# Kernel optimization log

Measured on AMD Instinct MI355X. Metric: run time of the kernel, lower is better.

The kernel has to match this reference:

```python
import jax, jax.numpy as jnp
import numpy as np

N_NODES = 256
BATCH = 1024
N_LAYERS = 2  # total linear layers = N_LAYERS + 1, each followed by tanh


def setup_inputs() -> dict:
    key = jax.random.key(0)
    ks = jax.random.split(key, 4)
    scale = 1.0 / np.sqrt(N_NODES)
    x = jax.random.normal(ks[0], (BATCH, N_NODES), dtype=jnp.float32)
    # nn.Linear weights: [out_features, in_features], no bias
    W0 = jax.random.normal(ks[1], (N_NODES, N_NODES), dtype=jnp.float32) * scale
    W1 = jax.random.normal(ks[2], (N_NODES, N_NODES), dtype=jnp.float32) * scale
    W2 = jax.random.normal(ks[3], (N_NODES, N_NODES), dtype=jnp.float32) * scale
    return {"x": x, "W0": W0, "W1": W1, "W2": W2}


def reference(x, W0, W1, W2):
    # Original loop: for each node i, zero out column i of x (x @ Par with
    # Par = I - e_i e_i^T), run the 3-layer tanh MLP, keep output column i.
    # Vectorized: build all N masked copies at once.
    N = x.shape[1]
    mask = (1.0 - jnp.eye(N, dtype=x.dtype))  # [i, j]: zero col j==i
    Xm = x[None, :, :] * mask[:, None, :]     # [N, B, N]
    # nn.Linear: y = h @ W.T ; tanh after every layer (incl. last)
    h = jnp.tanh(jnp.einsum('ibn,mn->ibm', Xm, W0))
    h = jnp.tanh(jnp.einsum('ibn,mn->ibm', h, W1))
    h = jnp.tanh(jnp.einsum('ibn,mn->ibm', h, W2))  # [N, B, N]
    # f_x[b, i] = h[i, b, i]
    f_x = jnp.einsum('ibi->bi', h)
    return f_x
```

## Files before the change

kernel.cpp:

```cpp
#include <hip/hip_runtime.h>
#include <hip/hip_bf16.h>

#define N_NODES 256
#define BATCH   1024
#define ROWB    528
#define CSC     2.8853900817779268f

typedef __attribute__((ext_vector_type(8))) short bf16x8;
typedef __attribute__((ext_vector_type(4))) float f32x4;
typedef __attribute__((ext_vector_type(2))) float f32x2;

__device__ __forceinline__ float ftanh(float x) {
    float e = __builtin_amdgcn_exp2f(x * CSC);
    float r = __builtin_amdgcn_rcpf(e + 1.0f);
    return fmaf(-2.0f, r, 1.0f);
}

__device__ __forceinline__ unsigned short f2bf(float f) {
    unsigned u = __float_as_uint(f);
    return (unsigned short)((u + 0x7fffu + ((u >> 16) & 1u)) >> 16);
}

__device__ __forceinline__ unsigned pack_bf2(float a, float b) {
    union { __hip_bfloat162 h; unsigned u; } cvt;
    cvt.h = __float22bfloat162_rn(make_float2(a, b));
    return cvt.u;
}

__device__ __forceinline__ f32x2 pkfma(f32x2 a, f32x2 b, f32x2 c) {
    return __builtin_elementwise_fma(a, b, c);
}

__device__ __forceinline__ f32x2 tanh2_pre(f32x2 d2) {
    f32x2 e2;
    e2.x = __builtin_amdgcn_exp2f(d2.x);
    e2.y = __builtin_amdgcn_exp2f(d2.y);
    e2 = e2 + 1.0f;
    f32x2 r2;
    r2.x = __builtin_amdgcn_rcpf(e2.x);
    r2.y = __builtin_amdgcn_rcpf(e2.y);
    return pkfma((f32x2){-2.f, -2.f}, r2, (f32x2){1.f, 1.f});
}

template <int CTRL>
__device__ __forceinline__ float dpp_add(float s) {
    int t = __builtin_amdgcn_update_dpp(0, __float_as_int(s), CTRL, 0xf, 0xf, true);
    return s + __int_as_float(t);
}

__global__ void z0_prep(const float* __restrict__ x, const float* __restrict__ W0,
                        const float* __restrict__ W1, float* __restrict__ Z0c,
                        float* __restrict__ xT, float* __restrict__ W0c,
                        unsigned short* __restrict__ W1bf) {
    __shared__ float xs[32][36];
    __shared__ float ws[32][36];
    int t = threadIdx.x;

    int gb = (blockIdx.y * 32 + blockIdx.x) * 256 + t;
    {
        int i = gb >> 8, m = gb & 255;
        W0c[gb]  = W0[m * 256 + i] * CSC;
        W1bf[gb] = f2bf(W1[gb] * CSC);
    }
#pragma unroll
    for (int r = 0; r < 4; ++r) {
        int id = r * 65536 + gb;
        int i = id >> 10, b = id & 1023;
        xT[id] = x[b * 256 + i];
    }

    int b0 = blockIdx.x * 32, m0 = blockIdx.y * 32;
    int lr = t >> 3, lc = (t & 7) << 2;
    int tr = (t >> 4) << 1, tc = (t & 15) << 1;
    float acc00 = 0.f, acc01 = 0.f, acc10 = 0.f, acc11 = 0.f;
    for (int k0 = 0; k0 < 256; k0 += 32) {
        *(float4*)&xs[lr][lc] = *(const float4*)&x[(b0 + lr) * 256 + k0 + lc];
        *(float4*)&ws[lr][lc] = *(const float4*)&W0[(m0 + lr) * 256 + k0 + lc];
        __syncthreads();
#pragma unroll
        for (int k = 0; k < 32; ++k) {
            float a0 = xs[tr][k], a1 = xs[tr + 1][k];
            float w0v = ws[tc][k], w1v = ws[tc + 1][k];
            acc00 = fmaf(a0, w0v, acc00);
            acc01 = fmaf(a0, w1v, acc01);
            acc10 = fmaf(a1, w0v, acc10);
            acc11 = fmaf(a1, w1v, acc11);
        }
        __syncthreads();
    }
    Z0c[(b0 + tr) * 256 + m0 + tc]         = acc00 * CSC;
    Z0c[(b0 + tr) * 256 + m0 + tc + 1]     = acc01 * CSC;
    Z0c[(b0 + tr + 1) * 256 + m0 + tc]     = acc10 * CSC;
    Z0c[(b0 + tr + 1) * 256 + m0 + tc + 1] = acc11 * CSC;
}

__launch_bounds__(256, 4)
__global__ void fused(const float* __restrict__ Z0c, const float* __restrict__ xT,
                      const float* __restrict__ W0c,
                      const unsigned short* __restrict__ W1bf,
                      const float* __restrict__ W2, float* __restrict__ out) {
    __shared__ __align__(16) unsigned char h0s[64 * ROWB];
    __shared__ float wavepart[4 * 64];
    const int t  = threadIdx.x;
    const int r0 = blockIdx.x * 64;
    const int i  = blockIdx.y;

    const int wave = t >> 6, lane = t & 63;
    const int lr = lane & 15, lh = lane >> 4;

    float w2v[4];
#pragma unroll
    for (int nt = 0; nt < 4; ++nt)
        w2v[nt] = W2[i * 256 + wave * 64 + nt * 16 + lr];

    {
        const int rowgrp = t >> 5, chunk = t & 31;
        const int col0 = chunk << 3;
        unsigned char* wbase = h0s + rowgrp * ROWB + chunk * 16;
        f32x2 wv[4];
        {
            float4 w0a = *(const float4*)&W0c[i * 256 + col0];
            float4 w0b = *(const float4*)&W0c[i * 256 + col0 + 4];
            wv[0] = (f32x2){w0a.x, w0a.y};
            wv[1] = (f32x2){w0a.z, w0a.w};
            wv[2] = (f32x2){w0b.x, w0b.y};
            wv[3] = (f32x2){w0b.z, w0b.w};
        }
#pragma unroll
        for (int p = 0; p < 8; ++p) {
            int row = p * 8 + rowgrp;
            float xi = xT[i * 1024 + r0 + row];
            f32x2 nxi = (f32x2){-xi, -xi};
            float4 za = *(const float4*)&Z0c[(r0 + row) * 256 + col0];
            float4 zb = *(const float4*)&Z0c[(r0 + row) * 256 + col0 + 4];
            f32x2 zv[4] = {(f32x2){za.x, za.y}, (f32x2){za.z, za.w},
                           (f32x2){zb.x, zb.y}, (f32x2){zb.z, zb.w}};
            unsigned pk[4];
#pragma unroll
            for (int e = 0; e < 4; ++e) {
                f32x2 h = tanh2_pre(pkfma(nxi, wv[e], zv[e]));
                pk[e] = pack_bf2(h.x, h.y);
            }
            *(uint4*)(wbase + p * 8 * ROWB) = make_uint4(pk[0], pk[1], pk[2], pk[3]);
        }
    }
    __syncthreads();

    f32x4 acc[4][4];
#pragma unroll
    for (int a = 0; a < 4; ++a)
#pragma unroll
        for (int b = 0; b < 4; ++b)
            acc[a][b] = (f32x4){0.f, 0.f, 0.f, 0.f};

    const unsigned char* abase[4];
#pragma unroll
    for (int mt = 0; mt < 4; ++mt)
        abase[mt] = h0s + (mt * 16 + lr) * ROWB + lh * 16;

    const unsigned short* w1p[4];
#pragma unroll
    for (int nt = 0; nt < 4; ++nt)
        w1p[nt] = W1bf + (wave * 64 + nt * 16 + lr) * 256 + lh * 8;
    bf16x8 bnext[4];
#pragma unroll
    for (int nt = 0; nt < 4; ++nt)
        bnext[nt] = *(const bf16x8*)(w1p[nt]);

#pragma unroll
    for (int ks = 0; ks < 8; ++ks) {
        bf16x8 bfrag[4];
#pragma unroll
        for (int nt = 0; nt < 4; ++nt) {
            bfrag[nt] = bnext[nt];
            if (ks < 7)
                bnext[nt] = *(const bf16x8*)(w1p[nt] + (ks + 1) * 32);
        }
        bf16x8 afrag[4];
#pragma unroll
        for (int mt = 0; mt < 4; ++mt)
            afrag[mt] = *(const bf16x8*)(abase[mt] + ks * 64);
#pragma unroll
        for (int mt = 0; mt < 4; ++mt)
#pragma unroll
            for (int nt = 0; nt < 4; ++nt)
                acc[mt][nt] = __builtin_amdgcn_mfma_f32_16x16x32_bf16(
                    afrag[mt], bfrag[nt], acc[mt][nt], 0, 0, 0);
    }

#pragma unroll
    for (int mt = 0; mt < 4; ++mt) {
#pragma unroll
        for (int p = 0; p < 2; ++p) {
            f32x2 s2 = (f32x2){0.f, 0.f};
#pragma unroll
            for (int nt = 0; nt < 4; ++nt) {
                f32x2 zc = (f32x2){acc[mt][nt][2 * p], acc[mt][nt][2 * p + 1]};
                f32x2 h2 = tanh2_pre(zc);
                s2 = pkfma(h2, (f32x2){w2v[nt], w2v[nt]}, s2);
            }
#pragma unroll
            for (int q = 0; q < 2; ++q) {
                float s = s2[q];
                s = dpp_add<0x118>(s);
                s = dpp_add<0x114>(s);
                s = dpp_add<0x112>(s);
                s = dpp_add<0x111>(s);
                if (lr == 15)
                    wavepart[wave * 64 + mt * 16 + lh * 4 + 2 * p + q] = s;
            }
        }
    }
    __syncthreads();

    if (t < 64) {
        float s = wavepart[t] + wavepart[64 + t] + wavepart[128 + t] + wavepart[192 + t];
        out[(r0 + t) * 256 + i] = ftanh(s);
    }
}

extern "C" void kernel_launch(void* const* d_in, const int* in_sizes, int n_in,
                              void* d_out, int out_size, void* d_ws, size_t ws_size,
                              hipStream_t stream) {
    const float* x  = (const float*)d_in[0];
    const float* W0 = (const float*)d_in[1];
    const float* W1 = (const float*)d_in[2];
    const float* W2 = (const float*)d_in[3];
    float* out = (float*)d_out;

    char* ws = (char*)d_ws;
    float* Z0c           = (float*)ws;
    float* xT            = (float*)(ws + (1 << 20));
    float* W0c           = (float*)(ws + (2 << 20));
    unsigned short* W1bf = (unsigned short*)(ws + (2 << 20) + (256 << 10));

    z0_prep<<<dim3(32, 8), 256, 0, stream>>>(x, W0, W1, Z0c, xT, W0c, W1bf);
    fused<<<dim3(16, 256), 256, 0, stream>>>(Z0c, xT, W0c, W1bf, W2, out);
}
```

Measured before the change: 87.78 us.

## Warp-specialize fused kernel: producer waves build h0 while MFMA waves consume

The fused kernel now processes 8 node indices per block with 512 threads. Four producer waves compute the tanh-masked first layer into a double-buffered LDS tile for the next index, while four consumer waves run the MFMA second layer and the reduction for the current index. The final output write for each index is deferred by one iteration. The goal is to overlap the elementwise/global-load phase with the matrix phase and to amortize block launch. The costs are more LDS per block, a block-wide barrier per index, and a lower occupancy bound.

```diff
diff --git a/kernel.cpp b/kernel.cpp
--- a/kernel.cpp
+++ b/kernel.cpp
@@ -3,6 +3,7 @@
 
 #define N_NODES 256
 #define BATCH   1024
+#define NI      8
 #define ROWB    528
 #define CSC     2.8853900817779268f
 
@@ -94,42 +95,30 @@
     Z0c[(b0 + tr + 1) * 256 + m0 + tc + 1] = acc11 * CSC;
 }
 
-__launch_bounds__(256, 4)
+__launch_bounds__(512, 2)
 __global__ void fused(const float* __restrict__ Z0c, const float* __restrict__ xT,
                       const float* __restrict__ W0c,
                       const unsigned short* __restrict__ W1bf,
                       const float* __restrict__ W2, float* __restrict__ out) {
-    __shared__ __align__(16) unsigned char h0s[64 * ROWB];
-    __shared__ float wavepart[4 * 64];
+    __shared__ __align__(16) unsigned char h0buf[2][64 * ROWB];
+    __shared__ float wavepart[2][4 * 64];
     const int t  = threadIdx.x;
     const int r0 = blockIdx.x * 64;
-    const int i  = blockIdx.y;
-
-    const int wave = t >> 6, lane = t & 63;
-    const int lr = lane & 15, lh = lane >> 4;
-
-    float w2v[4];
-#pragma unroll
-    for (int nt = 0; nt < 4; ++nt)
-        w2v[nt] = W2[i * 256 + wave * 64 + nt * 16 + lr];
-
-    {
-        const int rowgrp = t >> 5, chunk = t & 31;
-        const int col0 = chunk << 3;
-        unsigned char* wbase = h0s + rowgrp * ROWB + chunk * 16;
-        f32x2 wv[4];
-        {
-            float4 w0a = *(const float4*)&W0c[i * 256 + col0];
-            float4 w0b = *(const float4*)&W0c[i * 256 + col0 + 4];
-            wv[0] = (f32x2){w0a.x, w0a.y};
-            wv[1] = (f32x2){w0a.z, w0a.w};
-            wv[2] = (f32x2){w0b.x, w0b.y};
-            wv[3] = (f32x2){w0b.z, w0b.w};
-        }
+    const int i0 = blockIdx.y * NI;
+    const int wid = t >> 6;
+
+    if (wid >= 4) {
+        const int pt = t & 255;
+        const int rowgrp = pt >> 5, chunk = pt & 31, col0 = chunk << 3;
+        unsigned char* wbase = h0buf[0] + rowgrp * ROWB + chunk * 16;
+        float4 w0a = *(const float4*)&W0c[i0 * 256 + col0];
+        float4 w0b = *(const float4*)&W0c[i0 * 256 + col0 + 4];
+        f32x2 wv[4] = {(f32x2){w0a.x, w0a.y}, (f32x2){w0a.z, w0a.w},
+                       (f32x2){w0b.x, w0b.y}, (f32x2){w0b.z, w0b.w}};
 #pragma unroll
         for (int p = 0; p < 8; ++p) {
             int row = p * 8 + rowgrp;
-            float xi = xT[i * 1024 + r0 + row];
+            float xi = xT[i0 * 1024 + r0 + row];
             f32x2 nxi = (f32x2){-xi, -xi};
             float4 za = *(const float4*)&Z0c[(r0 + row) * 256 + col0];
             float4 zb = *(const float4*)&Z0c[(r0 + row) * 256 + col0 + 4];
@@ -146,76 +135,124 @@
     }
     __syncthreads();
 
-    f32x4 acc[4][4];
-#pragma unroll
-    for (int a = 0; a < 4; ++a)
-#pragma unroll
-        for (int b = 0; b < 4; ++b)
-            acc[a][b] = (f32x4){0.f, 0.f, 0.f, 0.f};
-
-    const unsigned char* abase[4];
-#pragma unroll
-    for (int mt = 0; mt < 4; ++mt)
-        abase[mt] = h0s + (mt * 16 + lr) * ROWB + lh * 16;
-
-    const unsigned short* w1p[4];
-#pragma unroll
-    for (int nt = 0; nt < 4; ++nt)
-        w1p[nt] = W1bf + (wave * 64 + nt * 16 + lr) * 256 + lh * 8;
-    bf16x8 bnext[4];
-#pragma unroll
-    for (int nt = 0; nt < 4; ++nt)
-        bnext[nt] = *(const bf16x8*)(w1p[nt]);
-
-#pragma unroll
-    for (int ks = 0; ks < 8; ++ks) {
-        bf16x8 bfrag[4];
-#pragma unroll
-        for (int nt = 0; nt < 4; ++nt) {
-            bfrag[nt] = bnext[nt];
-            if (ks < 7)
-                bnext[nt] = *(const bf16x8*)(w1p[nt] + (ks + 1) * 32);
+    for (int k = 0; k < NI; ++k) {
+        const int i = i0 + k;
+        if (wid < 4) {
+            const int lane = t & 63, lr = lane & 15, lh = lane >> 4;
+            float w2v[4];
+#pragma unroll
+            for (int nt = 0; nt < 4; ++nt)
+                w2v[nt] = W2[i * 256 + wid * 64 + nt * 16 + lr];
+
+            f32x4 acc[4][4];
+#pragma unroll
+            for (int a = 0; a < 4; ++a)
+#pragma unroll
+                for (int b = 0; b < 4; ++b)
+                    acc[a][b] = (f32x4){0.f, 0.f, 0.f, 0.f};
+
+            const unsigned char* abase[4];
+#pragma unroll
+            for (int mt = 0; mt < 4; ++mt)
+                abase[mt] = h0buf[k & 1] + (mt * 16 + lr) * ROWB + lh * 16;
+
+            const unsigned short* w1p[4];
+#pragma unroll
+            for (int nt = 0; nt < 4; ++nt)
+                w1p[nt] = W1bf + (wid * 64 + nt * 16 + lr) * 256 + lh * 8;
+            bf16x8 bnext[4];
+#pragma unroll
+            for (int nt = 0; nt < 4; ++nt)
+                bnext[nt] = *(const bf16x8*)(w1p[nt]);
+
+#pragma unroll
+            for (int ks = 0; ks < 8; ++ks) {
+                bf16x8 bfrag[4];
+#pragma unroll
+                for (int nt = 0; nt < 4; ++nt) {
+                    bfrag[nt] = bnext[nt];
+                    if (ks < 7)
+                        bnext[nt] = *(const bf16x8*)(w1p[nt] + (ks + 1) * 32);
+                }
+                bf16x8 afrag[4];
+#pragma unroll
+                for (int mt = 0; mt < 4; ++mt)
+                    afrag[mt] = *(const bf16x8*)(abase[mt] + ks * 64);
+#pragma unroll
+                for (int mt = 0; mt < 4; ++mt)
+#pragma unroll
+                    for (int nt = 0; nt < 4; ++nt)
+                        acc[mt][nt] = __builtin_amdgcn_mfma_f32_16x16x32_bf16(
+                            afrag[mt], bfrag[nt], acc[mt][nt], 0, 0, 0);
+            }
+
+#pragma unroll
+            for (int mt = 0; mt < 4; ++mt) {
+#pragma unroll
+                for (int p = 0; p < 2; ++p) {
+                    f32x2 s2 = (f32x2){0.f, 0.f};
+#pragma unroll
+                    for (int nt = 0; nt < 4; ++nt) {
+                        f32x2 zc = (f32x2){acc[mt][nt][2 * p], acc[mt][nt][2 * p + 1]};
+                        f32x2 h2 = tanh2_pre(zc);
+                        s2 = pkfma(h2, (f32x2){w2v[nt], w2v[nt]}, s2);
+                    }
+#pragma unroll
+                    for (int q = 0; q < 2; ++q) {
+                        float s = s2[q];
+                        s = dpp_add<0x118>(s);
+                        s = dpp_add<0x114>(s);
+                        s = dpp_add<0x112>(s);
+                        s = dpp_add<0x111>(s);
+                        if (lr == 15)
+                            wavepart[k & 1][wid * 64 + mt * 16 + lh * 4 + 2 * p + q] = s;
+                    }
+                }
+            }
+        } else {
+            if (k + 1 < NI) {
+                const int inx = i + 1;
+                const int pt = t & 255;
+                const int rowgrp = pt >> 5, chunk = pt & 31, col0 = chunk << 3;
+                unsigned char* wbase = h0buf[(k + 1) & 1] + rowgrp * ROWB + chunk * 16;
+                float4 w0a = *(const float4*)&W0c[inx * 256 + col0];
+                float4 w0b = *(const float4*)&W0c[inx * 256 + col0 + 4];
+                f32x2 wv[4] = {(f32x2){w0a.x, w0a.y}, (f32x2){w0a.z, w0a.w},
+                               (f32x2){w0b.x, w0b.y}, (f32x2){w0b.z, w0b.w}};
+#pragma unroll
+                for (int p = 0; p < 8; ++p) {
+                    int row = p * 8 + rowgrp;
+                    float xi = xT[inx * 1024 + r0 + row];
+                    f32x2 nxi = (f32x2){-xi, -xi};
+                    float4 za = *(const float4*)&Z0c[(r0 + row) * 256 + col0];
+                    float4 zb = *(const float4*)&Z0c[(r0 + row) * 256 + col0 + 4];
+                    f32x2 zv[4] = {(f32x2){za.x, za.y}, (f32x2){za.z, za.w},
+                                   (f32x2){zb.x, zb.y}, (f32x2){zb.z, zb.w}};
+                    unsigned pk[4];
+#pragma unroll
+                    for (int e = 0; e < 4; ++e) {
+                        f32x2 h = tanh2_pre(pkfma(nxi, wv[e], zv[e]));
+                        pk[e] = pack_bf2(h.x, h.y);
+                    }
+                    *(uint4*)(wbase + p * 8 * ROWB) =
+                        make_uint4(pk[0], pk[1], pk[2], pk[3]);
+                }
+            }
+            if (k > 0 && t < 320) {
+                const int l = t - 256;
+                const float* wp = wavepart[(k + 1) & 1];
+                float s = wp[l] + wp[64 + l] + wp[128 + l] + wp[192 + l];
+                out[(r0 + l) * 256 + (i - 1)] = ftanh(s);
+            }
         }
-        bf16x8 afrag[4];
-#pragma unroll
-        for (int mt = 0; mt < 4; ++mt)
-            afrag[mt] = *(const bf16x8*)(abase[mt] + ks * 64);
-#pragma unroll
-        for (int mt = 0; mt < 4; ++mt)
-#pragma unroll
-            for (int nt = 0; nt < 4; ++nt)
-                acc[mt][nt] = __builtin_amdgcn_mfma_f32_16x16x32_bf16(
-                    afrag[mt], bfrag[nt], acc[mt][nt], 0, 0, 0);
-    }
-
-#pragma unroll
-    for (int mt = 0; mt < 4; ++mt) {
-#pragma unroll
-        for (int p = 0; p < 2; ++p) {
-            f32x2 s2 = (f32x2){0.f, 0.f};
-#pragma unroll
-            for (int nt = 0; nt < 4; ++nt) {
-                f32x2 zc = (f32x2){acc[mt][nt][2 * p], acc[mt][nt][2 * p + 1]};
-                f32x2 h2 = tanh2_pre(zc);
-                s2 = pkfma(h2, (f32x2){w2v[nt], w2v[nt]}, s2);
-            }
-#pragma unroll
-            for (int q = 0; q < 2; ++q) {
-                float s = s2[q];
-                s = dpp_add<0x118>(s);
-                s = dpp_add<0x114>(s);
-                s = dpp_add<0x112>(s);
-                s = dpp_add<0x111>(s);
-                if (lr == 15)
-                    wavepart[wave * 64 + mt * 16 + lh * 4 + 2 * p + q] = s;
-            }
-        }
-    }
-    __syncthreads();
-
-    if (t < 64) {
-        float s = wavepart[t] + wavepart[64 + t] + wavepart[128 + t] + wavepart[192 + t];
-        out[(r0 + t) * 256 + i] = ftanh(s);
+        __syncthreads();
+    }
+
+    if (t >= 256 && t < 320) {
+        const int l = t - 256;
+        const float* wp = wavepart[(NI - 1) & 1];
+        float s = wp[l] + wp[64 + l] + wp[128 + l] + wp[192 + l];
+        out[(r0 + l) * 256 + (i0 + NI - 1)] = ftanh(s);
     }
 }
 
@@ -235,5 +272,5 @@
     unsigned short* W1bf = (unsigned short*)(ws + (2 << 20) + (256 << 10));
 
     z0_prep<<<dim3(32, 8), 256, 0, stream>>>(x, W0, W1, Z0c, xT, W0c, W1bf);
-    fused<<<dim3(16, 256), 256, 0, stream>>>(Z0c, xT, W0c, W1bf, W2, out);
-}
+    fused<<<dim3(16, 256 / NI), 512, 0, stream>>>(Z0c, xT, W0c, W1bf, W2, out);
+}
```

Result: slower. 110.0 us (+25.3%).

## Swizzle LDS h0 layout, hoist global loads ahead of tanh compute

Applied to the files above, without the earlier changes.

Replaces the padded 528-byte LDS row stride with a 512-byte stride and an XOR swizzle of 16-byte chunks by row, to avoid bank conflicts without padding. It also moves the W1 fragment prefetch and all Z0/xT/W0 global loads ahead of the first-layer tanh so their latency overlaps, and lowers launch bounds from 4 to 3 blocks per SIMD to leave more registers. The extra preloaded registers may reduce occupancy. A redundant first afrag load loop remains but is overwritten and likely eliminated by the compiler.

```diff
diff --git a/kernel.cpp b/kernel.cpp
--- a/kernel.cpp
+++ b/kernel.cpp
@@ -3,7 +3,6 @@
 
 #define N_NODES 256
 #define BATCH   1024
-#define ROWB    528
 #define CSC     2.8853900817779268f
 
 typedef __attribute__((ext_vector_type(8))) short bf16x8;
@@ -94,12 +93,12 @@
     Z0c[(b0 + tr + 1) * 256 + m0 + tc + 1] = acc11 * CSC;
 }
 
-__launch_bounds__(256, 4)
+__launch_bounds__(256, 3)
 __global__ void fused(const float* __restrict__ Z0c, const float* __restrict__ xT,
                       const float* __restrict__ W0c,
                       const unsigned short* __restrict__ W1bf,
                       const float* __restrict__ W2, float* __restrict__ out) {
-    __shared__ __align__(16) unsigned char h0s[64 * ROWB];
+    __shared__ __align__(16) unsigned char h0s[64 * 512];
     __shared__ float wavepart[4 * 64];
     const int t  = threadIdx.x;
     const int r0 = blockIdx.x * 64;
@@ -113,35 +112,46 @@
     for (int nt = 0; nt < 4; ++nt)
         w2v[nt] = W2[i * 256 + wave * 64 + nt * 16 + lr];
 
+    const unsigned short* w1p[4];
+#pragma unroll
+    for (int nt = 0; nt < 4; ++nt)
+        w1p[nt] = W1bf + (wave * 64 + nt * 16 + lr) * 256 + lh * 8;
+    bf16x8 bnext[4];
+#pragma unroll
+    for (int nt = 0; nt < 4; ++nt)
+        bnext[nt] = *(const bf16x8*)(w1p[nt]);
+
+    const int rowgrp = t >> 5, chunk = t & 31, col0 = chunk << 3;
+    float4 w0a = *(const float4*)&W0c[i * 256 + col0];
+    float4 w0b = *(const float4*)&W0c[i * 256 + col0 + 4];
+
+    float xi[8];
+    float4 za[8], zb[8];
+#pragma unroll
+    for (int p = 0; p < 8; ++p) {
+        int row = p * 8 + rowgrp;
+        xi[p] = xT[i * 1024 + r0 + row];
+        za[p] = *(const float4*)&Z0c[(r0 + row) * 256 + col0];
+        zb[p] = *(const float4*)&Z0c[(r0 + row) * 256 + col0 + 4];
+    }
+
     {
-        const int rowgrp = t >> 5, chunk = t & 31;
-        const int col0 = chunk << 3;
-        unsigned char* wbase = h0s + rowgrp * ROWB + chunk * 16;
-        f32x2 wv[4];
-        {
-            float4 w0a = *(const float4*)&W0c[i * 256 + col0];
-            float4 w0b = *(const float4*)&W0c[i * 256 + col0 + 4];
-            wv[0] = (f32x2){w0a.x, w0a.y};
-            wv[1] = (f32x2){w0a.z, w0a.w};
-            wv[2] = (f32x2){w0b.x, w0b.y};
-            wv[3] = (f32x2){w0b.z, w0b.w};
-        }
+        f32x2 wv[4] = {(f32x2){w0a.x, w0a.y}, (f32x2){w0a.z, w0a.w},
+                       (f32x2){w0b.x, w0b.y}, (f32x2){w0b.z, w0b.w}};
 #pragma unroll
         for (int p = 0; p < 8; ++p) {
             int row = p * 8 + rowgrp;
-            float xi = xT[i * 1024 + r0 + row];
-            f32x2 nxi = (f32x2){-xi, -xi};
-            float4 za = *(const float4*)&Z0c[(r0 + row) * 256 + col0];
-            float4 zb = *(const float4*)&Z0c[(r0 + row) * 256 + col0 + 4];
-            f32x2 zv[4] = {(f32x2){za.x, za.y}, (f32x2){za.z, za.w},
-                           (f32x2){zb.x, zb.y}, (f32x2){zb.z, zb.w}};
+            f32x2 nxi = (f32x2){-xi[p], -xi[p]};
+            f32x2 zv[4] = {(f32x2){za[p].x, za[p].y}, (f32x2){za[p].z, za[p].w},
+                           (f32x2){zb[p].x, zb[p].y}, (f32x2){zb[p].z, zb[p].w}};
             unsigned pk[4];
 #pragma unroll
             for (int e = 0; e < 4; ++e) {
                 f32x2 h = tanh2_pre(pkfma(nxi, wv[e], zv[e]));
                 pk[e] = pack_bf2(h.x, h.y);
             }
-            *(uint4*)(wbase + p * 8 * ROWB) = make_uint4(pk[0], pk[1], pk[2], pk[3]);
+            *(uint4*)(h0s + row * 512 + (((chunk ^ (row & 31)) << 4))) =
+                make_uint4(pk[0], pk[1], pk[2], pk[3]);
         }
     }
     __syncthreads();
@@ -153,22 +163,9 @@
         for (int b = 0; b < 4; ++b)
             acc[a][b] = (f32x4){0.f, 0.f, 0.f, 0.f};
 
-    const unsigned char* abase[4];
-#pragma unroll
-    for (int mt = 0; mt < 4; ++mt)
-        abase[mt] = h0s + (mt * 16 + lr) * ROWB + lh * 16;
-
-    const unsigned short* w1p[4];
-#pragma unroll
-    for (int nt = 0; nt < 4; ++nt)
-        w1p[nt] = W1bf + (wave * 64 + nt * 16 + lr) * 256 + lh * 8;
-    bf16x8 bnext[4];
-#pragma unroll
-    for (int nt = 0; nt < 4; ++nt)
-        bnext[nt] = *(const bf16x8*)(w1p[nt]);
-
 #pragma unroll
     for (int ks = 0; ks < 8; ++ks) {
+        int kchunk = ks * 4 + (lh >> 1);
         bf16x8 bfrag[4];
 #pragma unroll
         for (int nt = 0; nt < 4; ++nt) {
@@ -178,8 +175,18 @@
         }
         bf16x8 afrag[4];
 #pragma unroll
-        for (int mt = 0; mt < 4; ++mt)
-            afrag[mt] = *(const bf16x8*)(abase[mt] + ks * 64);
+        for (int mt = 0; mt < 4; ++mt) {
+            int row = mt * 16 + lr;
+            afrag[mt] = *(const bf16x8*)(h0s + row * 512 +
+                                         ((kchunk ^ (row & 31)) << 4) +
+                                         ((lh & 1) ? 0 : 0));
+        }
+#pragma unroll
+        for (int mt = 0; mt < 4; ++mt) {
+            int row = mt * 16 + lr;
+            int ch2 = ks * 4 + lh;
+            afrag[mt] = *(const bf16x8*)(h0s + row * 512 + ((ch2 ^ (row & 31)) << 4));
+        }
 #pragma unroll
         for (int mt = 0; mt < 4; ++mt)
 #pragma unroll
```

Result: no change. 88.61 us (+0.9%).

## Halve fused-kernel row tile to 32 and XOR-swizzle the h0 LDS layout

Applied to the files above, without the earlier changes.

Cuts the batch rows handled per block from 64 to 32, doubling the grid to 32x256 blocks and halving the accumulators and LDS each block needs. The padded LDS rows are replaced with an XOR swizzle on the 16-byte chunk index to avoid bank conflicts without padding. Each block now reloads all of W1 for only half as many rows, so W1 and W0 traffic per unit of work doubles in exchange for more occupancy and parallelism.

```diff
diff --git a/kernel.cpp b/kernel.cpp
--- a/kernel.cpp
+++ b/kernel.cpp
@@ -3,7 +3,7 @@
 
 #define N_NODES 256
 #define BATCH   1024
-#define ROWB    528
+#define ROWS    32
 #define CSC     2.8853900817779268f
 
 typedef __attribute__((ext_vector_type(8))) short bf16x8;
@@ -99,10 +99,10 @@
                       const float* __restrict__ W0c,
                       const unsigned short* __restrict__ W1bf,
                       const float* __restrict__ W2, float* __restrict__ out) {
-    __shared__ __align__(16) unsigned char h0s[64 * ROWB];
-    __shared__ float wavepart[4 * 64];
+    __shared__ __align__(16) unsigned char h0s[ROWS * 512];
+    __shared__ float wavepart[4 * ROWS];
     const int t  = threadIdx.x;
-    const int r0 = blockIdx.x * 64;
+    const int r0 = blockIdx.x * ROWS;
     const int i  = blockIdx.y;
 
     const int wave = t >> 6, lane = t & 63;
@@ -116,7 +116,6 @@
     {
         const int rowgrp = t >> 5, chunk = t & 31;
         const int col0 = chunk << 3;
-        unsigned char* wbase = h0s + rowgrp * ROWB + chunk * 16;
         f32x2 wv[4];
         {
             float4 w0a = *(const float4*)&W0c[i * 256 + col0];
@@ -127,7 +126,7 @@
             wv[3] = (f32x2){w0b.z, w0b.w};
         }
 #pragma unroll
-        for (int p = 0; p < 8; ++p) {
+        for (int p = 0; p < 4; ++p) {
             int row = p * 8 + rowgrp;
             float xi = xT[i * 1024 + r0 + row];
             f32x2 nxi = (f32x2){-xi, -xi};
@@ -141,22 +140,18 @@
                 f32x2 h = tanh2_pre(pkfma(nxi, wv[e], zv[e]));
                 pk[e] = pack_bf2(h.x, h.y);
             }
-            *(uint4*)(wbase + p * 8 * ROWB) = make_uint4(pk[0], pk[1], pk[2], pk[3]);
+            *(uint4*)(h0s + row * 512 + ((chunk ^ row) << 4)) =
+                make_uint4(pk[0], pk[1], pk[2], pk[3]);
         }
     }
     __syncthreads();
 
-    f32x4 acc[4][4];
-#pragma unroll
-    for (int a = 0; a < 4; ++a)
+    f32x4 acc[2][4];
+#pragma unroll
+    for (int a = 0; a < 2; ++a)
 #pragma unroll
         for (int b = 0; b < 4; ++b)
             acc[a][b] = (f32x4){0.f, 0.f, 0.f, 0.f};
-
-    const unsigned char* abase[4];
-#pragma unroll
-    for (int mt = 0; mt < 4; ++mt)
-        abase[mt] = h0s + (mt * 16 + lr) * ROWB + lh * 16;
 
     const unsigned short* w1p[4];
 #pragma unroll
@@ -176,12 +171,15 @@
             if (ks < 7)
                 bnext[nt] = *(const bf16x8*)(w1p[nt] + (ks + 1) * 32);
         }
-        bf16x8 afrag[4];
-#pragma unroll
-        for (int mt = 0; mt < 4; ++mt)
-            afrag[mt] = *(const bf16x8*)(abase[mt] + ks * 64);
-#pragma unroll
-        for (int mt = 0; mt < 4; ++mt)
+        bf16x8 afrag[2];
+#pragma unroll
+        for (int mt = 0; mt < 2; ++mt) {
+            int row = mt * 16 + lr;
+            int ch2 = ks * 4 + lh;
+            afrag[mt] = *(const bf16x8*)(h0s + row * 512 + ((ch2 ^ row) << 4));
+        }
+#pragma unroll
+        for (int mt = 0; mt < 2; ++mt)
 #pragma unroll
             for (int nt = 0; nt < 4; ++nt)
                 acc[mt][nt] = __builtin_amdgcn_mfma_f32_16x16x32_bf16(
@@ -189,7 +187,7 @@
     }
 
 #pragma unroll
-    for (int mt = 0; mt < 4; ++mt) {
+    for (int mt = 0; mt < 2; ++mt) {
 #pragma unroll
         for (int p = 0; p < 2; ++p) {
             f32x2 s2 = (f32x2){0.f, 0.f};
@@ -207,14 +205,15 @@
                 s = dpp_add<0x112>(s);
                 s = dpp_add<0x111>(s);
                 if (lr == 15)
-                    wavepart[wave * 64 + mt * 16 + lh * 4 + 2 * p + q] = s;
+                    wavepart[wave * ROWS + mt * 16 + lh * 4 + 2 * p + q] = s;
             }
         }
     }
     __syncthreads();
 
-    if (t < 64) {
-        float s = wavepart[t] + wavepart[64 + t] + wavepart[128 + t] + wavepart[192 + t];
+    if (t < ROWS) {
+        float s = wavepart[t] + wavepart[ROWS + t] +
+                  wavepart[2 * ROWS + t] + wavepart[3 * ROWS + t];
         out[(r0 + t) * 256 + i] = ftanh(s);
     }
 }
@@ -235,5 +234,5 @@
     unsigned short* W1bf = (unsigned short*)(ws + (2 << 20) + (256 << 10));
 
     z0_prep<<<dim3(32, 8), 256, 0, stream>>>(x, W0, W1, Z0c, xT, W0c, W1bf);
-    fused<<<dim3(16, 256), 256, 0, stream>>>(Z0c, xT, W0c, W1bf, W2, out);
-}
+    fused<<<dim3(BATCH / ROWS, 256), 256, 0, stream>>>(Z0c, xT, W0c, W1bf, W2, out);
+}
```

New measurement: 141.5 us. 61.2% more time.
